# Performance work log

Measured on AMD Instinct MI355X. Metric: run time of the kernel, lower is better.

Reference implementation:

```python
import jax, jax.numpy as jnp
import numpy as np

N = 50000      # nodes
E = 400000     # edges per relation
R = 3          # edge types
D = 128        # input_dim == hidden_dim
H = 8          # attention heads
Dh = D // H    # per-head dim (16)
OUT = 1        # output logits
NEG_SLOPE = 0.2
LN_EPS = 1e-5


def setup_inputs() -> dict:
    key = jax.random.key(0)
    ks = jax.random.split(key, 20)
    s = 0.05
    f32 = jnp.float32
    return {
        "feat": jax.random.normal(ks[0], (N, D), f32),
        "edge_src": jax.random.randint(ks[1], (R, E), 0, N, dtype=jnp.int32),
        "edge_dst": jax.random.randint(ks[2], (R, E), 0, N, dtype=jnp.int32),
        # conv1: per-relation GATConv params (W, attn_l, attn_r, bias)
        "W1": jax.random.normal(ks[3], (R, D, H * Dh), f32) * s,
        "al1": jax.random.normal(ks[4], (R, H, Dh), f32) * s,
        "ar1": jax.random.normal(ks[5], (R, H, Dh), f32) * s,
        "b1": jnp.zeros((R, H * Dh), f32),
        # conv2
        "W2": jax.random.normal(ks[6], (R, D, H * Dh), f32) * s,
        "al2": jax.random.normal(ks[7], (R, H, Dh), f32) * s,
        "ar2": jax.random.normal(ks[8], (R, H, Dh), f32) * s,
        "b2": jnp.zeros((R, H * Dh), f32),
        # LayerNorm
        "ln_g": jnp.ones((D,), f32),
        "ln_b": jnp.zeros((D,), f32),
        # classifier MLP (dropout inactive at eval)
        "Wc1": jax.random.normal(ks[9], (D, D), f32) * s,
        "bc1": jnp.zeros((D,), f32),
        "Wc2": jax.random.normal(ks[10], (D, OUT), f32) * s,
        "bc2": jnp.zeros((OUT,), f32),
    }


def _gat(x, src, dst, W, al, ar, b):
    """DGL GATConv on one relation: x [N,Din] -> [N, H*Dh]."""
    h = (x @ W).reshape(N, H, Dh)                       # projected feats
    el = (h * al).sum(-1)                               # [N,H] src attn term
    er = (h * ar).sum(-1)                               # [N,H] dst attn term
    e = jax.nn.leaky_relu(el[src] + er[dst], NEG_SLOPE)  # [E,H]
    # edge-softmax over incoming edges per dst node, per head
    m = jax.ops.segment_max(e, dst, num_segments=N)     # [N,H]
    ex = jnp.exp(e - m[dst])
    denom = jax.ops.segment_sum(ex, dst, num_segments=N)
    alpha = ex / denom[dst]                             # [E,H]
    msg = alpha[:, :, None] * h[src]                    # [E,H,Dh]
    out = jax.ops.segment_sum(msg, dst, num_segments=N)  # [N,H,Dh]
    return out.reshape(N, H * Dh) + b


def _hetero(x, edge_src, edge_dst, W, al, ar, b):
    out = jnp.zeros((N, H * Dh), x.dtype)
    for r in range(R):  # small fixed relation count
        out = out + _gat(x, edge_src[r], edge_dst[r], W[r], al[r], ar[r], b[r])
    return out


def reference(feat, edge_src, edge_dst, W1, al1, ar1, b1, W2, al2, ar2, b2,
              ln_g, ln_b, Wc1, bc1, Wc2, bc2):
    h1 = jax.nn.relu(_hetero(feat, edge_src, edge_dst, W1, al1, ar1, b1))
    h2 = _hetero(h1, edge_src, edge_dst, W2, al2, ar2, b2)
    h = h2 + h1
    mu = h.mean(-1, keepdims=True)
    var = ((h - mu) ** 2).mean(-1, keepdims=True)
    h = (h - mu) * jax.lax.rsqrt(var + LN_EPS) * ln_g + ln_b
    h = jax.nn.relu(h @ Wc1 + bc1)
    return h @ Wc2 + bc2
```

## Files before the change

### kernel.cpp

```cpp
#include <hip/hip_runtime.h>
#include <math.h>

#define NN 50000
#define NE 400000
#define NREL 3
#define NCH 196

typedef __bf16 bf16x8 __attribute__((ext_vector_type(8)));
typedef float floatx4 __attribute__((ext_vector_type(4)));

__device__ __forceinline__ unsigned short f2bf(float f) {
  unsigned int u = __float_as_uint(f);
  return (unsigned short)((u + 0x7fffu + ((u >> 16) & 1u)) >> 16);
}

__global__ __launch_bounds__(256) void prep_wt(
    const float* __restrict__ W1, const float* __restrict__ W2,
    const float* __restrict__ Wc1, unsigned short* __restrict__ Wt) {
  int mat = blockIdx.x >> 3, slab = blockIdx.x & 7;
  const float* Wsrc = mat < 3 ? W1 + mat * 16384
                    : (mat < 6 ? W2 + (mat - 3) * 16384 : Wc1);
  unsigned short* dst = Wt + (size_t)mat * 144 * 128;
  int k0 = slab * 16;
#pragma unroll
  for (int i = 0; i < 8; ++i) {
    int idx = i * 256 + threadIdx.x;
    int k = k0 + (idx >> 7), nn = idx & 127;
    dst[nn * 128 + k] = f2bf(Wsrc[k * 128 + nn]);
  }
}

__global__ __launch_bounds__(256) void prep_attn(
    const float* __restrict__ W1, const float* __restrict__ W2,
    const float* __restrict__ al1, const float* __restrict__ ar1,
    const float* __restrict__ al2, const float* __restrict__ ar2,
    unsigned short* __restrict__ Wt) {
  int mat = blockIdx.x;
  const float* Wsrc = mat < 3 ? W1 + mat * 16384 : W2 + (mat - 3) * 16384;
  const float* alp = mat < 3 ? al1 + mat * 128 : al2 + (mat - 3) * 128;
  const float* arp = mat < 3 ? ar1 + mat * 128 : ar2 + (mat - 3) * 128;
  unsigned short* dst = Wt + (size_t)mat * 144 * 128;
#pragma unroll
  for (int i = 0; i < 8; ++i) {
    int j = i * 256 + threadIdx.x;
    int half = j >> 10, jj = j & 1023;
    int k = jj >> 3, h = jj & 7;
    const float* av = half ? arp : alp;
    float s = 0.f;
#pragma unroll
    for (int d = 0; d < 16; ++d) s += Wsrc[k * 128 + h * 16 + d] * av[h * 16 + d];
    dst[(128 + half * 8 + h) * 128 + k] = f2bf(s);
  }
}

__global__ __launch_bounds__(256) void gemm3_attn_mfma(
    const float* __restrict__ X, const unsigned short* __restrict__ Wt,
    unsigned short* __restrict__ hp, float* __restrict__ el,
    float* __restrict__ er, int n) {
  __shared__ unsigned short Xs[64 * 136];
  __shared__ unsigned short Ws[144 * 136];
  int t = threadIdx.x;
  int rowbase = blockIdx.x * 64;

  const float4* X4 = (const float4*)X;
#pragma unroll
  for (int i = 0; i < 8; ++i) {
    int v = t + i * 256;
    int row = v >> 5, k4 = (v & 31) * 4;
    float4 x = make_float4(0.f, 0.f, 0.f, 0.f);
    if (rowbase + row < n) x = X4[(size_t)(rowbase + row) * 32 + (v & 31)];
    ushort4 p;
    p.x = f2bf(x.x); p.y = f2bf(x.y); p.z = f2bf(x.z); p.w = f2bf(x.w);
    *(ushort4*)&Xs[row * 136 + k4] = p;
  }

  int lane = t & 63, wave = t >> 6;
  int quad = lane >> 4, l = lane & 15;

  for (int r = 0; r < NREL; ++r) {
    __syncthreads();
    const uint4* WtR = (const uint4*)(Wt + (size_t)r * 144 * 128);
#pragma unroll
    for (int i = 0; i < 9; ++i) {
      int v = t + i * 256;
      ((uint4*)Ws)[(v >> 4) * 17 + (v & 15)] = WtR[v];
    }
    __syncthreads();

    floatx4 acc[9];
#pragma unroll
    for (int i = 0; i < 9; ++i) acc[i] = floatx4{0.f, 0.f, 0.f, 0.f};
#pragma unroll
    for (int ks = 0; ks < 4; ++ks) {
      bf16x8 a = *(const bf16x8*)&Xs[(wave * 16 + l) * 136 + ks * 32 + quad * 8];
#pragma unroll
      for (int nt = 0; nt < 9; ++nt) {
        bf16x8 b = *(const bf16x8*)&Ws[(nt * 16 + l) * 136 + ks * 32 + quad * 8];
        acc[nt] = __builtin_amdgcn_mfma_f32_16x16x32_bf16(a, b, acc[nt], 0, 0, 0);
      }
    }

    unsigned short* hpR = hp + (size_t)r * NN * 128;
    float* elR = el + (size_t)r * NN * 8;
    float* erR = er + (size_t)r * NN * 8;
    int r0 = rowbase + wave * 16 + quad * 4;
#pragma unroll
    for (int reg = 0; reg < 4; ++reg) {
      int row = r0 + reg;
      if (row < n) {
#pragma unroll
        for (int nt = 0; nt < 8; ++nt)
          hpR[(size_t)row * 128 + nt * 16 + l] = f2bf(acc[nt][reg]);
        if (l < 8) elR[row * 8 + l] = acc[8][reg];
        else       erR[row * 8 + (l - 8)] = acc[8][reg];
      }
    }
  }
}

__global__ __launch_bounds__(256) void gemm_head_mfma(
    const float* __restrict__ X, const unsigned short* __restrict__ Wt,
    const float* __restrict__ bc1, const float* __restrict__ wc2,
    const float* __restrict__ bc2, float* __restrict__ out, int n) {
  __shared__ unsigned short Xs[64 * 136];
  __shared__ unsigned short Ws[128 * 136];
  int t = threadIdx.x;
  int rowbase = blockIdx.x * 64;

  const float4* X4 = (const float4*)X;
#pragma unroll
  for (int i = 0; i < 8; ++i) {
    int v = t + i * 256;
    int row = v >> 5, k4 = (v & 31) * 4;
    float4 x = make_float4(0.f, 0.f, 0.f, 0.f);
    if (rowbase + row < n) x = X4[(size_t)(rowbase + row) * 32 + (v & 31)];
    ushort4 p;
    p.x = f2bf(x.x); p.y = f2bf(x.y); p.z = f2bf(x.z); p.w = f2bf(x.w);
    *(ushort4*)&Xs[row * 136 + k4] = p;
  }
  const uint4* WtR = (const uint4*)Wt;
#pragma unroll
  for (int i = 0; i < 8; ++i) {
    int v = t + i * 256;
    ((uint4*)Ws)[(v >> 4) * 17 + (v & 15)] = WtR[v];
  }
  __syncthreads();

  int lane = t & 63, wave = t >> 6;
  int quad = lane >> 4, l = lane & 15;

  floatx4 acc[8];
#pragma unroll
  for (int i = 0; i < 8; ++i) acc[i] = floatx4{0.f, 0.f, 0.f, 0.f};
#pragma unroll
  for (int ks = 0; ks < 4; ++ks) {
    bf16x8 a = *(const bf16x8*)&Xs[(wave * 16 + l) * 136 + ks * 32 + quad * 8];
#pragma unroll
    for (int nt = 0; nt < 8; ++nt) {
      bf16x8 b = *(const bf16x8*)&Ws[(nt * 16 + l) * 136 + ks * 32 + quad * 8];
      acc[nt] = __builtin_amdgcn_mfma_f32_16x16x32_bf16(a, b, acc[nt], 0, 0, 0);
    }
  }

  float bv[8], wv[8];
#pragma unroll
  for (int nt = 0; nt < 8; ++nt) {
    bv[nt] = bc1[nt * 16 + l];
    wv[nt] = wc2[nt * 16 + l];
  }
  int r0 = rowbase + wave * 16 + quad * 4;
#pragma unroll
  for (int reg = 0; reg < 4; ++reg) {
    float s = 0.f;
#pragma unroll
    for (int nt = 0; nt < 8; ++nt)
      s += fmaxf(acc[nt][reg] + bv[nt], 0.f) * wv[nt];
    s += __shfl_xor(s, 1); s += __shfl_xor(s, 2);
    s += __shfl_xor(s, 4); s += __shfl_xor(s, 8);
    int row = r0 + reg;
    if (l == 0 && row < n) out[row] = s + bc2[0];
  }
}

__global__ __launch_bounds__(256) void hist_kernel(
    const int* __restrict__ edst, int* __restrict__ cnt, int* __restrict__ rank) {
  int t = blockIdx.x * 256 + threadIdx.x;
  if (t >= NREL * NE) return;
  int r = t / NE;
  rank[t] = atomicAdd(&cnt[r * NN + edst[t]], 1);
}

__global__ __launch_bounds__(256) void scan1(
    const int* __restrict__ cnt, int* __restrict__ partials) {
  __shared__ int s[256];
  int r = blockIdx.x / NCH, c = blockIdx.x % NCH;
  int i = c * 256 + threadIdx.x;
  s[threadIdx.x] = (i < NN) ? cnt[r * NN + i] : 0;
  __syncthreads();
  for (int off = 128; off; off >>= 1) {
    if (threadIdx.x < off) s[threadIdx.x] += s[threadIdx.x + off];
    __syncthreads();
  }
  if (threadIdx.x == 0) partials[r * NCH + c] = s[0];
}

__global__ __launch_bounds__(256) void scan2(int* __restrict__ partials) {
  __shared__ int s[256];
  int r = blockIdx.x;
  int t = threadIdx.x;
  int v = (t < NCH) ? partials[r * NCH + t] : 0;
  s[t] = v;
  __syncthreads();
  for (int off = 1; off < 256; off <<= 1) {
    int x = (t >= off) ? s[t - off] : 0;
    __syncthreads();
    s[t] += x;
    __syncthreads();
  }
  if (t < NCH) partials[r * NCH + t] = s[t] - v;
}

__global__ __launch_bounds__(256) void scan3(
    const int* __restrict__ cnt, const int* __restrict__ partials,
    int* __restrict__ rowptr) {
  __shared__ int s[256];
  int r = blockIdx.x / NCH, c = blockIdx.x % NCH;
  int t = threadIdx.x;
  int i = c * 256 + t;
  int v = (i < NN) ? cnt[r * NN + i] : 0;
  s[t] = v;
  __syncthreads();
  for (int off = 1; off < 256; off <<= 1) {
    int x = (t >= off) ? s[t - off] : 0;
    __syncthreads();
    s[t] += x;
    __syncthreads();
  }
  int base = partials[r * NCH + c];
  if (i < NN) rowptr[r * (NN + 1) + i] = base + s[t] - v;
  if (c == NCH - 1 && t == 0) rowptr[r * (NN + 1) + NN] = NE;
}

__global__ __launch_bounds__(256) void scatter_kernel(
    const int* __restrict__ esrc, const int* __restrict__ edst,
    const int* __restrict__ rowptr, const int* __restrict__ rank,
    int* __restrict__ col) {
  int t = blockIdx.x * 256 + threadIdx.x;
  if (t >= NREL * NE) return;
  int r = t / NE;
  int pos = rowptr[r * (NN + 1) + edst[t]] + rank[t];
  col[(size_t)r * NE + pos] = esrc[t];
}

__global__ __launch_bounds__(256) void gather_all(
    const int* __restrict__ rowptr, const int* __restrict__ col,
    const float* __restrict__ el, const float* __restrict__ er,
    const unsigned short* __restrict__ hp, const float* __restrict__ b,
    float* __restrict__ h1, const float* __restrict__ g,
    const float* __restrict__ beta, int mode) {
  int wid = (blockIdx.x * 256 + threadIdx.x) >> 6;
  int lane = threadIdx.x & 63;
  if (wid >= NN) return;
  int head = lane >> 3;
  int c = lane * 2;
  float ax = 0.f, ay = 0.f;
#pragma unroll
  for (int r = 0; r < NREL; ++r) {
    const int* rp = rowptr + r * (NN + 1);
    const int* cl = col + (size_t)r * NE;
    const float* elr = el + (size_t)r * NN * 8;
    const unsigned short* hpr = hp + (size_t)r * NN * 128;
    float er_d = er[(size_t)r * NN * 8 + wid * 8 + head];
    int start = rp[wid], end = rp[wid + 1];
    float den = 0.f, sx = 0.f, sy = 0.f;
    for (int i = start; i < end; i += 4) {
      int last = end - 1;
      int s0 = cl[i];
      int s1 = cl[min(i + 1, last)];
      int s2 = cl[min(i + 2, last)];
      int s3 = cl[min(i + 3, last)];
      float e0 = elr[s0 * 8 + head] + er_d;
      float e1 = elr[s1 * 8 + head] + er_d;
      float e2 = elr[s2 * 8 + head] + er_d;
      float e3 = elr[s3 * 8 + head] + er_d;
      unsigned int u0 = *(const unsigned int*)&hpr[(size_t)s0 * 128 + c];
      unsigned int u1 = *(const unsigned int*)&hpr[(size_t)s1 * 128 + c];
      unsigned int u2 = *(const unsigned int*)&hpr[(size_t)s2 * 128 + c];
      unsigned int u3 = *(const unsigned int*)&hpr[(size_t)s3 * 128 + c];
      e0 = (e0 > 0.f) ? e0 : 0.2f * e0;
      e1 = (e1 > 0.f) ? e1 : 0.2f * e1;
      e2 = (e2 > 0.f) ? e2 : 0.2f * e2;
      e3 = (e3 > 0.f) ? e3 : 0.2f * e3;
      float x0 = __expf(e0);
      float x1 = (i + 1 < end) ? __expf(e1) : 0.f;
      float x2 = (i + 2 < end) ? __expf(e2) : 0.f;
      float x3 = (i + 3 < end) ? __expf(e3) : 0.f;
      den += x0 + x1 + x2 + x3;
      sx += x0 * __uint_as_float(u0 << 16) + x1 * __uint_as_float(u1 << 16) +
            x2 * __uint_as_float(u2 << 16) + x3 * __uint_as_float(u3 << 16);
      sy += x0 * __uint_as_float(u0 & 0xffff0000u) +
            x1 * __uint_as_float(u1 & 0xffff0000u) +
            x2 * __uint_as_float(u2 & 0xffff0000u) +
            x3 * __uint_as_float(u3 & 0xffff0000u);
    }
    if (end > start) {
      float inv = 1.f / den;
      ax += sx * inv;
      ay += sy * inv;
    }
  }
  float bx = b[c] + b[128 + c] + b[256 + c];
  float by = b[c + 1] + b[128 + c + 1] + b[256 + c + 1];
  float2* hptr = (float2*)&h1[(size_t)wid * 128 + c];
  if (mode == 0) {
    *hptr = make_float2(fmaxf(ax + bx, 0.f), fmaxf(ay + by, 0.f));
  } else {
    float2 r1 = *hptr;
    float vx = ax + bx + r1.x;
    float vy = ay + by + r1.y;
    float s = vx + vy;
#pragma unroll
    for (int off = 32; off; off >>= 1) s += __shfl_xor(s, off);
    float mu = s * (1.f / 128.f);
    float dx = vx - mu, dy = vy - mu;
    float sq = dx * dx + dy * dy;
#pragma unroll
    for (int off = 32; off; off >>= 1) sq += __shfl_xor(sq, off);
    float rstd = rsqrtf(sq * (1.f / 128.f) + 1e-5f);
    *hptr = make_float2(dx * rstd * g[c] + beta[c],
                        dy * rstd * g[c + 1] + beta[c + 1]);
  }
}

extern "C" void kernel_launch(void* const* d_in, const int* in_sizes, int n_in,
                              void* d_out, int out_size, void* d_ws, size_t ws_size,
                              hipStream_t stream) {
  const float* feat = (const float*)d_in[0];
  const int* esrc = (const int*)d_in[1];
  const int* edst = (const int*)d_in[2];
  const float* W1 = (const float*)d_in[3];
  const float* al1 = (const float*)d_in[4];
  const float* ar1 = (const float*)d_in[5];
  const float* b1 = (const float*)d_in[6];
  const float* W2 = (const float*)d_in[7];
  const float* al2 = (const float*)d_in[8];
  const float* ar2 = (const float*)d_in[9];
  const float* b2 = (const float*)d_in[10];
  const float* lng = (const float*)d_in[11];
  const float* lnb = (const float*)d_in[12];
  const float* Wc1 = (const float*)d_in[13];
  const float* bc1 = (const float*)d_in[14];
  const float* Wc2 = (const float*)d_in[15];
  const float* bc2 = (const float*)d_in[16];
  float* out = (float*)d_out;

  unsigned short* hp = (unsigned short*)d_ws;
  float* el = (float*)(hp + (size_t)3 * NN * 128);
  float* er = el + (size_t)3 * NN * 8;
  float* h1 = er + (size_t)3 * NN * 8;
  int* rowptr = (int*)(h1 + (size_t)NN * 128);
  int* col = rowptr + NREL * (NN + 1);
  int* cnt = col + (size_t)NREL * NE;
  int* partials = cnt + NREL * NN;
  unsigned short* Wt = (unsigned short*)(((uintptr_t)(partials + NREL * NCH) + 15)
                                         & ~(uintptr_t)15);
  int* rank = (int*)el;

  const int gemm_grid = (NN + 63) / 64;
  const int edge_grid = (NREL * NE + 255) / 256;
  const int gg_grid = (NN * 64) / 256;

  prep_wt<<<56, 256, 0, stream>>>(W1, W2, Wc1, Wt);
  prep_attn<<<6, 256, 0, stream>>>(W1, W2, al1, ar1, al2, ar2, Wt);

  hipMemsetAsync(cnt, 0, (size_t)NREL * NN * sizeof(int), stream);
  hist_kernel<<<edge_grid, 256, 0, stream>>>(edst, cnt, rank);
  scan1<<<NREL * NCH, 256, 0, stream>>>(cnt, partials);
  scan2<<<NREL, 256, 0, stream>>>(partials);
  scan3<<<NREL * NCH, 256, 0, stream>>>(cnt, partials, rowptr);
  scatter_kernel<<<edge_grid, 256, 0, stream>>>(esrc, edst, rowptr, rank, col);

  gemm3_attn_mfma<<<gemm_grid, 256, 0, stream>>>(feat, Wt, hp, el, er, NN);
  gather_all<<<gg_grid, 256, 0, stream>>>(rowptr, col, el, er, hp, b1,
                                          h1, nullptr, nullptr, 0);
  gemm3_attn_mfma<<<gemm_grid, 256, 0, stream>>>(
      h1, Wt + (size_t)3 * 144 * 128, hp, el, er, NN);
  gather_all<<<gg_grid, 256, 0, stream>>>(rowptr, col, el, er, hp, b2,
                                          h1, lng, lnb, 1);
  gemm_head_mfma<<<gemm_grid, 256, 0, stream>>>(
      h1, Wt + (size_t)6 * 144 * 128, bc1, Wc2, bc2, out, NN);
}
```

Measured before the change: 395.9 us.

## Split gather wave across edges and heads, batch edge kernels four per thread

The gather kernel now assigns the 64 lanes of a wave to 8 edges × 8 heads for the exp computation. It then broadcasts each edge's weight and source via shuffles so that two half-waves each load 8-byte bf16 feature chunks for different edges. The per-head denominator is reduced across lanes and the two halves are combined before the bias, relu or LayerNorm epilogue. This replaces the older scheme, where every lane redundantly evaluated the attention for 4 edges, and is meant to raise memory-level parallelism and cut redundant el loads. The histogram and scatter kernels now process four edges per thread, issuing all loads before the atomics or stores. This adds shuffle overhead and wastes lanes when a node has few incoming edges.

Result: slower. 421.1 us (+6.4%).

```diff
diff --git a/kernel.cpp b/kernel.cpp
--- a/kernel.cpp
+++ b/kernel.cpp
@@ -5,6 +5,7 @@
 #define NE 400000
 #define NREL 3
 #define NCH 196
+#define EQ 300000
 
 typedef __bf16 bf16x8 __attribute__((ext_vector_type(8)));
 typedef float floatx4 __attribute__((ext_vector_type(4)));
@@ -185,9 +186,17 @@
 __global__ __launch_bounds__(256) void hist_kernel(
     const int* __restrict__ edst, int* __restrict__ cnt, int* __restrict__ rank) {
   int t = blockIdx.x * 256 + threadIdx.x;
-  if (t >= NREL * NE) return;
-  int r = t / NE;
-  rank[t] = atomicAdd(&cnt[r * NN + edst[t]], 1);
+  if (t >= EQ) return;
+  int d[4], r[4];
+#pragma unroll
+  for (int k = 0; k < 4; ++k) {
+    int tt = t + k * EQ;
+    d[k] = edst[tt];
+    r[k] = tt / NE;
+  }
+#pragma unroll
+  for (int k = 0; k < 4; ++k)
+    rank[t + k * EQ] = atomicAdd(&cnt[r[k] * NN + d[k]], 1);
 }
 
 __global__ __launch_bounds__(256) void scan1(
@@ -246,10 +255,19 @@
     const int* __restrict__ rowptr, const int* __restrict__ rank,
     int* __restrict__ col) {
   int t = blockIdx.x * 256 + threadIdx.x;
-  if (t >= NREL * NE) return;
-  int r = t / NE;
-  int pos = rowptr[r * (NN + 1) + edst[t]] + rank[t];
-  col[(size_t)r * NE + pos] = esrc[t];
+  if (t >= EQ) return;
+  int pos[4], s[4], r[4];
+#pragma unroll
+  for (int k = 0; k < 4; ++k) {
+    int tt = t + k * EQ;
+    r[k] = tt / NE;
+    int d = edst[tt];
+    s[k] = esrc[tt];
+    pos[k] = rowptr[r[k] * (NN + 1) + d] + rank[tt];
+  }
+#pragma unroll
+  for (int k = 0; k < 4; ++k)
+    col[(size_t)r[k] * NE + pos[k]] = s[k];
 }
 
 __global__ __launch_bounds__(256) void gather_all(
@@ -260,75 +278,82 @@
     const float* __restrict__ beta, int mode) {
   int wid = (blockIdx.x * 256 + threadIdx.x) >> 6;
   int lane = threadIdx.x & 63;
-  if (wid >= NN) return;
-  int head = lane >> 3;
-  int c = lane * 2;
-  float ax = 0.f, ay = 0.f;
+  int e1 = lane >> 3, h1_ = lane & 7;
+  int p = lane >> 5, d2 = lane & 31;
+  int h2 = d2 >> 2;
+  int sl0 = p * 8 + h2;
+
+  float ax = 0.f, ay = 0.f, az = 0.f, aw = 0.f;
 #pragma unroll
   for (int r = 0; r < NREL; ++r) {
     const int* rp = rowptr + r * (NN + 1);
     const int* cl = col + (size_t)r * NE;
     const float* elr = el + (size_t)r * NN * 8;
     const unsigned short* hpr = hp + (size_t)r * NN * 128;
-    float er_d = er[(size_t)r * NN * 8 + wid * 8 + head];
     int start = rp[wid], end = rp[wid + 1];
-    float den = 0.f, sx = 0.f, sy = 0.f;
-    for (int i = start; i < end; i += 4) {
-      int last = end - 1;
-      int s0 = cl[i];
-      int s1 = cl[min(i + 1, last)];
-      int s2 = cl[min(i + 2, last)];
-      int s3 = cl[min(i + 3, last)];
-      float e0 = elr[s0 * 8 + head] + er_d;
-      float e1 = elr[s1 * 8 + head] + er_d;
-      float e2 = elr[s2 * 8 + head] + er_d;
-      float e3 = elr[s3 * 8 + head] + er_d;
-      unsigned int u0 = *(const unsigned int*)&hpr[(size_t)s0 * 128 + c];
-      unsigned int u1 = *(const unsigned int*)&hpr[(size_t)s1 * 128 + c];
-      unsigned int u2 = *(const unsigned int*)&hpr[(size_t)s2 * 128 + c];
-      unsigned int u3 = *(const unsigned int*)&hpr[(size_t)s3 * 128 + c];
-      e0 = (e0 > 0.f) ? e0 : 0.2f * e0;
-      e1 = (e1 > 0.f) ? e1 : 0.2f * e1;
-      e2 = (e2 > 0.f) ? e2 : 0.2f * e2;
-      e3 = (e3 > 0.f) ? e3 : 0.2f * e3;
-      float x0 = __expf(e0);
-      float x1 = (i + 1 < end) ? __expf(e1) : 0.f;
-      float x2 = (i + 2 < end) ? __expf(e2) : 0.f;
-      float x3 = (i + 3 < end) ? __expf(e3) : 0.f;
-      den += x0 + x1 + x2 + x3;
-      sx += x0 * __uint_as_float(u0 << 16) + x1 * __uint_as_float(u1 << 16) +
-            x2 * __uint_as_float(u2 << 16) + x3 * __uint_as_float(u3 << 16);
-      sy += x0 * __uint_as_float(u0 & 0xffff0000u) +
-            x1 * __uint_as_float(u1 & 0xffff0000u) +
-            x2 * __uint_as_float(u2 & 0xffff0000u) +
-            x3 * __uint_as_float(u3 & 0xffff0000u);
+    if (end <= start) continue;
+    float er_d = er[(size_t)r * NN * 8 + wid * 8 + h1_];
+    float den = 0.f;
+    float rx = 0.f, ry = 0.f, rz = 0.f, rw = 0.f;
+    for (int base = start; base < end; base += 8) {
+      int idx = base + e1;
+      int s = cl[min(idx, end - 1)];
+      float e = elr[s * 8 + h1_] + er_d;
+      e = (e > 0.f) ? e : 0.2f * e;
+      float xv = (idx < end) ? __expf(e) : 0.f;
+      den += xv;
+      int nedge = end - base;
+#pragma unroll 4
+      for (int j = 0; 2 * j < nedge && j < 4; ++j) {
+        int srcl = sl0 + 16 * j;
+        float w = __shfl(xv, srcl);
+        int sj = __shfl(s, srcl);
+        uint2 u = *(const uint2*)&hpr[(size_t)sj * 128 + d2 * 4];
+        rx += w * __uint_as_float(u.x << 16);
+        ry += w * __uint_as_float(u.x & 0xffff0000u);
+        rz += w * __uint_as_float(u.y << 16);
+        rw += w * __uint_as_float(u.y & 0xffff0000u);
+      }
     }
-    if (end > start) {
-      float inv = 1.f / den;
-      ax += sx * inv;
-      ay += sy * inv;
-    }
-  }
-  float bx = b[c] + b[128 + c] + b[256 + c];
-  float by = b[c + 1] + b[128 + c + 1] + b[256 + c + 1];
-  float2* hptr = (float2*)&h1[(size_t)wid * 128 + c];
+    den += __shfl_xor(den, 8);
+    den += __shfl_xor(den, 16);
+    den += __shfl_xor(den, 32);
+    float inv = 1.f / __shfl(den, h2);
+    ax += rx * inv; ay += ry * inv; az += rz * inv; aw += rw * inv;
+  }
+  ax += __shfl_xor(ax, 32); ay += __shfl_xor(ay, 32);
+  az += __shfl_xor(az, 32); aw += __shfl_xor(aw, 32);
+
+  int c = d2 * 4;
+  float4 b0 = *(const float4*)&b[c];
+  float4 bb1 = *(const float4*)&b[128 + c];
+  float4 bb2 = *(const float4*)&b[256 + c];
+  float vx = ax + b0.x + bb1.x + bb2.x;
+  float vy = ay + b0.y + bb1.y + bb2.y;
+  float vz = az + b0.z + bb1.z + bb2.z;
+  float vw = aw + b0.w + bb1.w + bb2.w;
+  float4* hptr = (float4*)&h1[(size_t)wid * 128 + c];
   if (mode == 0) {
-    *hptr = make_float2(fmaxf(ax + bx, 0.f), fmaxf(ay + by, 0.f));
+    if (p == 0)
+      *hptr = make_float4(fmaxf(vx, 0.f), fmaxf(vy, 0.f),
+                          fmaxf(vz, 0.f), fmaxf(vw, 0.f));
   } else {
-    float2 r1 = *hptr;
-    float vx = ax + bx + r1.x;
-    float vy = ay + by + r1.y;
-    float s = vx + vy;
-#pragma unroll
-    for (int off = 32; off; off >>= 1) s += __shfl_xor(s, off);
+    float4 r1 = *hptr;
+    vx += r1.x; vy += r1.y; vz += r1.z; vw += r1.w;
+    float s = vx + vy + vz + vw;
+    s += __shfl_xor(s, 1); s += __shfl_xor(s, 2);
+    s += __shfl_xor(s, 4); s += __shfl_xor(s, 8); s += __shfl_xor(s, 16);
     float mu = s * (1.f / 128.f);
-    float dx = vx - mu, dy = vy - mu;
-    float sq = dx * dx + dy * dy;
-#pragma unroll
-    for (int off = 32; off; off >>= 1) sq += __shfl_xor(sq, off);
+    float dx = vx - mu, dy = vy - mu, dz = vz - mu, dw = vw - mu;
+    float sq = dx * dx + dy * dy + dz * dz + dw * dw;
+    sq += __shfl_xor(sq, 1); sq += __shfl_xor(sq, 2);
+    sq += __shfl_xor(sq, 4); sq += __shfl_xor(sq, 8); sq += __shfl_xor(sq, 16);
     float rstd = rsqrtf(sq * (1.f / 128.f) + 1e-5f);
-    *hptr = make_float2(dx * rstd * g[c] + beta[c],
-                        dy * rstd * g[c + 1] + beta[c + 1]);
+    float4 gv = *(const float4*)&g[c];
+    float4 bv = *(const float4*)&beta[c];
+    if (p == 0)
+      *hptr = make_float4(dx * rstd * gv.x + bv.x, dy * rstd * gv.y + bv.y,
+                          dz * rstd * gv.z + bv.z, dw * rstd * gv.w + bv.w);
   }
 }
 
@@ -367,7 +392,7 @@
   int* rank = (int*)el;
 
   const int gemm_grid = (NN + 63) / 64;
-  const int edge_grid = (NREL * NE + 255) / 256;
+  const int edge_grid = (EQ + 255) / 256;
   const int gg_grid = (NN * 64) / 256;
 
   prep_wt<<<56, 256, 0, stream>>>(W1, W2, Wc1, Wt);
```
